# Kernel tuning notes

Measured on AMD Instinct MI355X. Metric: run time of the kernel, lower is better.

Reference implementation:

```python
import jax, jax.numpy as jnp
import numpy as np

B, S, D = 4, 2048, 1024
H = 16
HD = D // H

def setup_inputs() -> dict:
    key = jax.random.key(0)
    ks = jax.random.split(key, 6)
    s = 0.02
    return {
        "input_tensor": jax.random.normal(ks[0], (B, S, D), dtype=jnp.float32),
        "Wq": jax.random.normal(ks[1], (D, D), dtype=jnp.float32) * s,
        "Wk": jax.random.normal(ks[2], (D, D), dtype=jnp.float32) * s,
        "Wv": jax.random.normal(ks[3], (D, D), dtype=jnp.float32) * s,
        "Wo": jax.random.normal(ks[4], (D, D), dtype=jnp.float32) * s,
        "bo": jax.random.normal(ks[5], (D,), dtype=jnp.float32) * s,
    }

def reference(input_tensor, Wq, Wk, Wv, Wo, bo):
    b, n, _ = input_tensor.shape
    # projections (nn.Linear: x @ W.T; bias=False for qkv)
    q = jnp.einsum('bnd,ed->bne', input_tensor, Wq).reshape(b, n, H, HD).transpose(0, 2, 1, 3)
    k = jnp.einsum('bnd,ed->bne', input_tensor, Wk).reshape(b, n, H, HD).transpose(0, 2, 1, 3)
    v = jnp.einsum('bnd,ed->bne', input_tensor, Wv).reshape(b, n, H, HD).transpose(0, 2, 1, 3)
    scores = jnp.einsum('bhqd,bhkd->bhqk', q, k)  # [B,H,S,S]
    causal = jnp.triu(jnp.ones((n, n), dtype=bool), k=1)
    scores = jnp.where(causal, -jnp.inf, scores)
    weights = jax.nn.softmax(scores / jnp.sqrt(jnp.float32(HD)), axis=-1)
    ctx = jnp.einsum('bhqk,bhkd->bhqd', weights, v)  # [B,H,S,HD]
    ctx = ctx.transpose(0, 2, 1, 3).reshape(b, n, D)
    return jnp.einsum('bnd,ed->bne', ctx, Wo) + bo
```

## Files before the change

### kernel.cpp

```cpp
#include <hip/hip_runtime.h>
#include <stdint.h>

#define S_LEN 2048
#define DIM   1024
#define NH    16
#define HD    64
#define BATCH 4
#define M_ROWS (BATCH * S_LEN)
#define PSTR  136

typedef __attribute__((ext_vector_type(8))) __bf16 bf16x8;
typedef __attribute__((ext_vector_type(4))) float  f32x4;

union Frag { bf16x8 v; uint4 q; };

__device__ __forceinline__ ushort f2bf(float f) {
  union { float f; unsigned u; } x; x.f = f;
  unsigned r = x.u + 0x7fffu + ((x.u >> 16) & 1u);
  return (ushort)(r >> 16);
}
__device__ __forceinline__ ushort f2bf_n(float f) {
  union { __bf16 b; ushort u; } x; x.b = (__bf16)f; return x.u;
}

__device__ __forceinline__ f32x4 mfma16(const Frag& a, const Frag& b, f32x4 c) {
  return __builtin_amdgcn_mfma_f32_16x16x32_bf16(a.v, b.v, c, 0, 0, 0);
}

__device__ __forceinline__ void gld_lds16(const ushort* g, ushort* l) {
  __builtin_amdgcn_global_load_lds(
      (__attribute__((address_space(1))) void*)g,
      (__attribute__((address_space(3))) void*)l, 16, 0, 0);
}

__global__ void cast_x_kernel(const float* __restrict__ src, ushort* __restrict__ dst) {
  int i = blockIdx.x * 256 + threadIdx.x;
  float4 f = ((const float4*)src)[i];
  ushort4 u; u.x = f2bf(f.x); u.y = f2bf(f.y); u.z = f2bf(f.z); u.w = f2bf(f.w);
  ((ushort4*)dst)[i] = u;
}

__global__ void cast_w_kernel(const float* __restrict__ w0, const float* __restrict__ w1,
                              const float* __restrict__ w2, const float* __restrict__ w3,
                              ushort* __restrict__ d0, ushort* __restrict__ d1,
                              ushort* __restrict__ d2, ushort* __restrict__ d3) {
  const float* s; ushort* d;
  int z = blockIdx.y;
  if (z == 0) { s = w0; d = d0; } else if (z == 1) { s = w1; d = d1; }
  else if (z == 2) { s = w2; d = d2; } else { s = w3; d = d3; }
  int i = blockIdx.x * 256 + threadIdx.x;
  float4 f = ((const float4*)s)[i];
  ushort4 u; u.x = f2bf(f.x); u.y = f2bf(f.y); u.z = f2bf(f.z); u.w = f2bf(f.w);
  ((ushort4*)d)[i] = u;
}

template <int MODE>
__global__ __launch_bounds__(256)
void gemm_bk64(const ushort* __restrict__ A,
               const ushort* __restrict__ B0, const ushort* __restrict__ B1,
               const ushort* __restrict__ B2,
               ushort* __restrict__ Qb, ushort* __restrict__ Kb, ushort* __restrict__ Vtb,
               float* __restrict__ outf, const float* __restrict__ bias, float scaleq) {
  __shared__ __align__(16) ushort As[128 * 64];
  __shared__ __align__(16) ushort Bs[128 * 64];
  const int K = DIM;
  int lane = threadIdx.x & 63, wave = threadIdx.x >> 6;
  int quad = lane >> 4, l15 = lane & 15;
  int rowBase = blockIdx.y * 128;
  int wsel, colBase;
  const ushort* Bt;
  if (MODE == 0) {
    wsel = blockIdx.x >> 3;
    colBase = (blockIdx.x & 7) * 128;
    Bt = (wsel == 0) ? B0 : (wsel == 1) ? B1 : B2;
  } else {
    wsel = 0;
    colBase = blockIdx.x * 128;
    Bt = B0;
  }
  int wm = (wave >> 1) * 64, wn = (wave & 1) * 64;

  const ushort* Ag = A + (size_t)rowBase * K;
  const ushort* Bg = Bt + (size_t)colBase * K;

  f32x4 acc[4][4];
#pragma unroll
  for (int i = 0; i < 4; i++)
#pragma unroll
    for (int j = 0; j < 4; j++) acc[i][j] = (f32x4){0.f, 0.f, 0.f, 0.f};

  for (int k0 = 0; k0 < K; k0 += 64) {
#pragma unroll
    for (int cc = 0; cc < 4; ++cc) {
      int c = wave * 4 + cc;
      int s = c * 64 + lane;
      int row = s >> 3;
      int c8 = (s & 7) ^ (row & 7);
      gld_lds16(Ag + (size_t)row * K + k0 + c8 * 8, &As[c * 512]);
      gld_lds16(Bg + (size_t)row * K + k0 + c8 * 8, &Bs[c * 512]);
    }
    __syncthreads();
    Frag af[4][2], bf[4][2];
#pragma unroll
    for (int t = 0; t < 4; t++) {
      int ar = wm + t * 16 + l15;
      int br = wn + t * 16 + l15;
#pragma unroll
      for (int kk = 0; kk < 2; kk++) {
        af[t][kk].q = *(const uint4*)&As[ar * 64 + (((kk * 4 + quad) ^ (ar & 7))) * 8];
        bf[t][kk].q = *(const uint4*)&Bs[br * 64 + (((kk * 4 + quad) ^ (br & 7))) * 8];
      }
    }
#pragma unroll
    for (int kk = 0; kk < 2; kk++)
#pragma unroll
      for (int i = 0; i < 4; i++)
#pragma unroll
        for (int j = 0; j < 4; j++) acc[i][j] = mfma16(af[i][kk], bf[j][kk], acc[i][j]);
    __syncthreads();
  }

#pragma unroll
  for (int i = 0; i < 4; i++) {
    int rowt = wm + i * 16 + quad * 4;
#pragma unroll
    for (int j = 0; j < 4; j++) {
      int e = colBase + wn + j * 16 + l15;
      if (MODE == 0) {
        int h = e >> 6, hd = e & 63;
        if (wsel < 2) {
          ushort* dst = wsel ? Kb : Qb;
          float sc = wsel ? 1.f : scaleq;
#pragma unroll
          for (int r = 0; r < 4; r++) {
            int m = rowBase + rowt + r;
            int b = m >> 11, s = m & (S_LEN - 1);
            dst[((size_t)((b * NH + h) * S_LEN + s) << 6) + hd] = f2bf(acc[i][j][r] * sc);
          }
        } else {
          int m0 = rowBase + rowt;
          int b = m0 >> 11, s0 = m0 & (S_LEN - 1);
          ushort4 u;
          u.x = f2bf(acc[i][j][0]); u.y = f2bf(acc[i][j][1]);
          u.z = f2bf(acc[i][j][2]); u.w = f2bf(acc[i][j][3]);
          *(ushort4*)&Vtb[((size_t)((b * NH + h) * HD + hd) << 11) + s0] = u;
        }
      } else {
        float bv = bias[e];
#pragma unroll
        for (int r = 0; r < 4; r++) {
          int m = rowBase + rowt + r;
          outf[(size_t)m * DIM + e] = acc[i][j][r] + bv;
        }
      }
    }
  }
}

__global__ __launch_bounds__(256)
void flash_attn(const ushort* __restrict__ Qb, const ushort* __restrict__ Kb,
                const ushort* __restrict__ Vtb, ushort* __restrict__ Ctx) {
  __shared__ __align__(16) ushort Ks[128 * 64];
  __shared__ __align__(16) ushort Vs[64 * 128];
  __shared__ __align__(16) ushort Ps[4][16 * PSTR];

  int lane = threadIdx.x & 63, wave = threadIdx.x >> 6;
  int quad = lane >> 4, l15 = lane & 15;
  int bh = blockIdx.x;
  int qt = (gridDim.y - 1) - blockIdx.y;
  int q0 = qt * 128, wq0 = wave * 32;

  const ushort* Qh = Qb + (size_t)bh * S_LEN * HD;
  const ushort* Kh = Kb + (size_t)bh * S_LEN * HD;
  const ushort* Vh = Vtb + (size_t)bh * HD * S_LEN;

#pragma unroll
  for (int cc = 0; cc < 4; ++cc) {
    int c = wave * 4 + cc;
    int s = c * 64 + lane;
    int row = s >> 3;
    int c8 = (s & 7) ^ (row & 7);
    gld_lds16(Qh + (size_t)(q0 + row) * HD + c8 * 8, &Ks[c * 512]);
  }
  __syncthreads();
  Frag qf[2][2];
#pragma unroll
  for (int it = 0; it < 2; ++it)
#pragma unroll
    for (int ks = 0; ks < 2; ++ks) {
      int row = wq0 + it * 16 + l15;
      int c8 = (ks * 4 + quad) ^ (row & 7);
      qf[it][ks].q = *(const uint4*)&Ks[row * 64 + c8 * 8];
    }
  __syncthreads();

  float lst[2] = {0.f, 0.f};
  f32x4 oacc[2][4];
#pragma unroll
  for (int it = 0; it < 2; ++it)
#pragma unroll
    for (int dt = 0; dt < 4; ++dt) oacc[it][dt] = (f32x4){0.f, 0.f, 0.f, 0.f};

  ushort* Pw = Ps[wave];

  for (int kt = 0; kt <= qt; ++kt) {
#pragma unroll
    for (int cc = 0; cc < 4; ++cc) {
      int c = wave * 4 + cc;
      int s = c * 64 + lane;
      int krow = s >> 3;
      int kc8 = (s & 7) ^ (krow & 7);
      gld_lds16(Kh + (size_t)(kt * 128 + krow) * HD + kc8 * 8, &Ks[c * 512]);
      int vrow = s >> 4;
      int vc8 = (s & 15) ^ (vrow & 15);
      gld_lds16(Vh + (size_t)vrow * S_LEN + kt * 128 + vc8 * 8, &Vs[c * 512]);
    }
    __syncthreads();

    f32x4 sacc[2][8];
#pragma unroll
    for (int jt = 0; jt < 8; ++jt) {
      int row = jt * 16 + l15;
      Frag kf0, kf1;
      kf0.q = *(const uint4*)&Ks[row * 64 + ((quad) ^ (row & 7)) * 8];
      kf1.q = *(const uint4*)&Ks[row * 64 + ((4 + quad) ^ (row & 7)) * 8];
#pragma unroll
      for (int it = 0; it < 2; ++it) {
        f32x4 a = (f32x4){0.f, 0.f, 0.f, 0.f};
        a = mfma16(kf0, qf[it][0], a);
        a = mfma16(kf1, qf[it][1], a);
        sacc[it][jt] = a;
      }
    }

    if (kt == qt) {
#pragma unroll
      for (int it = 0; it < 2; ++it)
#pragma unroll
        for (int jt = 0; jt < 8; ++jt)
#pragma unroll
          for (int r = 0; r < 4; ++r)
            if (jt * 16 + quad * 4 + r > wq0 + it * 16 + l15)
              sacc[it][jt][r] = -1e30f;
    }

#pragma unroll
    for (int it = 0; it < 2; ++it) {
      float ps = 0.f;
#pragma unroll
      for (int jt = 0; jt < 8; ++jt) {
        float p0 = exp2f(sacc[it][jt][0]);
        float p1 = exp2f(sacc[it][jt][1]);
        float p2 = exp2f(sacc[it][jt][2]);
        float p3 = exp2f(sacc[it][jt][3]);
        ps += (p0 + p1) + (p2 + p3);
        ushort4 u; u.x = f2bf_n(p0); u.y = f2bf_n(p1); u.z = f2bf_n(p2); u.w = f2bf_n(p3);
        *(ushort4*)&Pw[l15 * PSTR + jt * 16 + quad * 4] = u;
      }
      ps += __shfl_xor(ps, 16);
      ps += __shfl_xor(ps, 32);
      lst[it] += ps;

      Frag pf[4];
#pragma unroll
      for (int ks = 0; ks < 4; ++ks)
        pf[ks].q = *(const uint4*)&Pw[l15 * PSTR + ks * 32 + quad * 8];

#pragma unroll
      for (int dt = 0; dt < 4; ++dt) {
        f32x4 a = oacc[it][dt];
#pragma unroll
        for (int ks = 0; ks < 4; ++ks) {
          int row = dt * 16 + l15;
          Frag vf;
          vf.q = *(const uint4*)&Vs[row * 128 + (((ks * 4 + quad) ^ (row & 15))) * 8];
          a = mfma16(pf[ks], vf, a);
        }
        oacc[it][dt] = a;
      }
    }
    __syncthreads();
  }

  int b = bh >> 4, h = bh & 15;
#pragma unroll
  for (int it = 0; it < 2; ++it) {
    float linv = 1.f / lst[it];
    float lr[4];
#pragma unroll
    for (int r = 0; r < 4; ++r) lr[r] = __shfl(linv, quad * 4 + r);
#pragma unroll
    for (int r = 0; r < 4; ++r) {
      int qg = q0 + wq0 + it * 16 + quad * 4 + r;
      size_t base = ((size_t)(b * S_LEN + qg)) * DIM + h * HD;
#pragma unroll
      for (int dt = 0; dt < 4; ++dt)
        Ctx[base + dt * 16 + l15] = f2bf_n(oacc[it][dt][r] * lr[r]);
    }
  }
}

extern "C" void kernel_launch(void* const* d_in, const int* in_sizes, int n_in,
                              void* d_out, int out_size, void* d_ws, size_t ws_size,
                              hipStream_t stream) {
  (void)in_sizes; (void)n_in; (void)out_size; (void)ws_size;
  const float* x  = (const float*)d_in[0];
  const float* Wq = (const float*)d_in[1];
  const float* Wk = (const float*)d_in[2];
  const float* Wv = (const float*)d_in[3];
  const float* Wo = (const float*)d_in[4];
  const float* bo = (const float*)d_in[5];
  float* out = (float*)d_out;

  ushort* Xb  = (ushort*)d_ws;
  ushort* Wqb = Xb  + (size_t)M_ROWS * DIM;
  ushort* Wkb = Wqb + (size_t)DIM * DIM;
  ushort* Wvb = Wkb + (size_t)DIM * DIM;
  ushort* Wob = Wvb + (size_t)DIM * DIM;
  ushort* Qb  = Wob + (size_t)DIM * DIM;
  ushort* Kb  = Qb  + (size_t)M_ROWS * DIM;
  ushort* Vtb = Kb  + (size_t)M_ROWS * DIM;
  ushort* Ctx = Vtb + (size_t)M_ROWS * DIM;

  const float SCALE_Q = 0.18033688011112042f;

  cast_x_kernel<<<dim3(M_ROWS * DIM / 1024), 256, 0, stream>>>(x, Xb);
  cast_w_kernel<<<dim3(DIM * DIM / 1024, 4), 256, 0, stream>>>(Wq, Wk, Wv, Wo, Wqb, Wkb, Wvb, Wob);

  gemm_bk64<0><<<dim3(24, 64), 256, 0, stream>>>(Xb, Wqb, Wkb, Wvb, Qb, Kb, Vtb,
                                                 nullptr, nullptr, SCALE_Q);

  flash_attn<<<dim3(BATCH * NH, S_LEN / 128), 256, 0, stream>>>(Qb, Kb, Vtb, Ctx);

  gemm_bk64<1><<<dim3(8, 64), 256, 0, stream>>>(Ctx, Wob, nullptr, nullptr, nullptr, nullptr,
                                                nullptr, out, bo, 1.0f);
}
```

Measured before the change: 271.5 us.

## Double-buffer K/V tiles in flash attention and prefetch next tile during compute

K and V tiles now live in two LDS buffers. The next tile's global-to-LDS loads are issued before computing on the current one, which removes one barrier per iteration and hides load latency behind the MFMA work. The P scratch buffer switches from row padding to an XOR swizzle. V fragments are loaded once per dt and reused across both query sub-tiles, and s_setprio is raised around the MFMA sections. The added buffers raise LDS use to about 80KB per block, and launch_bounds now asks for 2 blocks per CU, which can squeeze the register budget.

```diff
diff --git a/kernel.cpp b/kernel.cpp
--- a/kernel.cpp
+++ b/kernel.cpp
@@ -7,7 +7,6 @@
 #define HD    64
 #define BATCH 4
 #define M_ROWS (BATCH * S_LEN)
-#define PSTR  136
 
 typedef __attribute__((ext_vector_type(8))) __bf16 bf16x8;
 typedef __attribute__((ext_vector_type(4))) float  f32x4;
@@ -157,12 +156,12 @@
   }
 }
 
-__global__ __launch_bounds__(256)
+__global__ __launch_bounds__(256, 2)
 void flash_attn(const ushort* __restrict__ Qb, const ushort* __restrict__ Kb,
                 const ushort* __restrict__ Vtb, ushort* __restrict__ Ctx) {
-  __shared__ __align__(16) ushort Ks[128 * 64];
-  __shared__ __align__(16) ushort Vs[64 * 128];
-  __shared__ __align__(16) ushort Ps[4][16 * PSTR];
+  __shared__ __align__(16) ushort Ks[2][128 * 64];
+  __shared__ __align__(16) ushort Vs[2][64 * 128];
+  __shared__ __align__(16) ushort Ps[4][16 * 128];
 
   int lane = threadIdx.x & 63, wave = threadIdx.x >> 6;
   int quad = lane >> 4, l15 = lane & 15;
@@ -178,11 +177,14 @@
   for (int cc = 0; cc < 4; ++cc) {
     int c = wave * 4 + cc;
     int s = c * 64 + lane;
-    int row = s >> 3;
-    int c8 = (s & 7) ^ (row & 7);
-    gld_lds16(Qh + (size_t)(q0 + row) * HD + c8 * 8, &Ks[c * 512]);
+    int krow = s >> 3, kc8 = (s & 7) ^ (krow & 7);
+    int vrow = s >> 4, vc8 = (s & 15) ^ (vrow & 15);
+    gld_lds16(Qh + (size_t)(q0 + krow) * HD + kc8 * 8, &Ks[1][c * 512]);
+    gld_lds16(Kh + (size_t)krow * HD + kc8 * 8, &Ks[0][c * 512]);
+    gld_lds16(Vh + (size_t)vrow * S_LEN + vc8 * 8, &Vs[0][c * 512]);
   }
   __syncthreads();
+
   Frag qf[2][2];
 #pragma unroll
   for (int it = 0; it < 2; ++it)
@@ -190,7 +192,7 @@
     for (int ks = 0; ks < 2; ++ks) {
       int row = wq0 + it * 16 + l15;
       int c8 = (ks * 4 + quad) ^ (row & 7);
-      qf[it][ks].q = *(const uint4*)&Ks[row * 64 + c8 * 8];
+      qf[it][ks].q = *(const uint4*)&Ks[1][row * 64 + c8 * 8];
     }
   __syncthreads();
 
@@ -202,28 +204,32 @@
     for (int dt = 0; dt < 4; ++dt) oacc[it][dt] = (f32x4){0.f, 0.f, 0.f, 0.f};
 
   ushort* Pw = Ps[wave];
-
+  const int psw = (l15 & 7) << 3;
+
+  int cur = 0;
   for (int kt = 0; kt <= qt; ++kt) {
-#pragma unroll
-    for (int cc = 0; cc < 4; ++cc) {
-      int c = wave * 4 + cc;
-      int s = c * 64 + lane;
-      int krow = s >> 3;
-      int kc8 = (s & 7) ^ (krow & 7);
-      gld_lds16(Kh + (size_t)(kt * 128 + krow) * HD + kc8 * 8, &Ks[c * 512]);
-      int vrow = s >> 4;
-      int vc8 = (s & 15) ^ (vrow & 15);
-      gld_lds16(Vh + (size_t)vrow * S_LEN + kt * 128 + vc8 * 8, &Vs[c * 512]);
-    }
-    __syncthreads();
+    if (kt < qt) {
+#pragma unroll
+      for (int cc = 0; cc < 4; ++cc) {
+        int c = wave * 4 + cc;
+        int s = c * 64 + lane;
+        int krow = s >> 3, kc8 = (s & 7) ^ (krow & 7);
+        int vrow = s >> 4, vc8 = (s & 15) ^ (vrow & 15);
+        gld_lds16(Kh + (size_t)((kt + 1) * 128 + krow) * HD + kc8 * 8, &Ks[cur ^ 1][c * 512]);
+        gld_lds16(Vh + (size_t)vrow * S_LEN + (kt + 1) * 128 + vc8 * 8, &Vs[cur ^ 1][c * 512]);
+      }
+    }
+    const ushort* Kc = Ks[cur];
+    const ushort* Vc = Vs[cur];
 
     f32x4 sacc[2][8];
+    __builtin_amdgcn_s_setprio(1);
 #pragma unroll
     for (int jt = 0; jt < 8; ++jt) {
       int row = jt * 16 + l15;
       Frag kf0, kf1;
-      kf0.q = *(const uint4*)&Ks[row * 64 + ((quad) ^ (row & 7)) * 8];
-      kf1.q = *(const uint4*)&Ks[row * 64 + ((4 + quad) ^ (row & 7)) * 8];
+      kf0.q = *(const uint4*)&Kc[row * 64 + ((quad ^ (row & 7))) * 8];
+      kf1.q = *(const uint4*)&Kc[row * 64 + (((4 + quad) ^ (row & 7))) * 8];
 #pragma unroll
       for (int it = 0; it < 2; ++it) {
         f32x4 a = (f32x4){0.f, 0.f, 0.f, 0.f};
@@ -232,6 +238,7 @@
         sacc[it][jt] = a;
       }
     }
+    __builtin_amdgcn_s_setprio(0);
 
     if (kt == qt) {
 #pragma unroll
@@ -244,6 +251,7 @@
               sacc[it][jt][r] = -1e30f;
     }
 
+    Frag pf[2][4];
 #pragma unroll
     for (int it = 0; it < 2; ++it) {
       float ps = 0.f;
@@ -255,31 +263,36 @@
         float p3 = exp2f(sacc[it][jt][3]);
         ps += (p0 + p1) + (p2 + p3);
         ushort4 u; u.x = f2bf_n(p0); u.y = f2bf_n(p1); u.z = f2bf_n(p2); u.w = f2bf_n(p3);
-        *(ushort4*)&Pw[l15 * PSTR + jt * 16 + quad * 4] = u;
+        *(ushort4*)&Pw[l15 * 128 + ((jt * 16 + quad * 4) ^ psw)] = u;
       }
       ps += __shfl_xor(ps, 16);
       ps += __shfl_xor(ps, 32);
       lst[it] += ps;
-
-      Frag pf[4];
 #pragma unroll
       for (int ks = 0; ks < 4; ++ks)
-        pf[ks].q = *(const uint4*)&Pw[l15 * PSTR + ks * 32 + quad * 8];
-
-#pragma unroll
-      for (int dt = 0; dt < 4; ++dt) {
+        pf[it][ks].q = *(const uint4*)&Pw[l15 * 128 + ((ks * 32 + quad * 8) ^ psw)];
+    }
+
+    __builtin_amdgcn_s_setprio(1);
+#pragma unroll
+    for (int dt = 0; dt < 4; ++dt) {
+      int row = dt * 16 + l15;
+      Frag vf[4];
+#pragma unroll
+      for (int ks = 0; ks < 4; ++ks)
+        vf[ks].q = *(const uint4*)&Vc[row * 128 + (((ks * 4 + quad) ^ (row & 15))) * 8];
+#pragma unroll
+      for (int it = 0; it < 2; ++it) {
         f32x4 a = oacc[it][dt];
 #pragma unroll
-        for (int ks = 0; ks < 4; ++ks) {
-          int row = dt * 16 + l15;
-          Frag vf;
-          vf.q = *(const uint4*)&Vs[row * 128 + (((ks * 4 + quad) ^ (row & 15))) * 8];
-          a = mfma16(pf[ks], vf, a);
-        }
+        for (int ks = 0; ks < 4; ++ks) a = mfma16(pf[it][ks], vf[ks], a);
         oacc[it][dt] = a;
       }
     }
+    __builtin_amdgcn_s_setprio(0);
+
     __syncthreads();
+    cur ^= 1;
   }
 
   int b = bh >> 4, h = bh & 15;
```

Result: faster. 256.1 us (-5.7%).

## Replace LDS round-trip for P with in-register permlane swaps and reorder tiles

Applied to the files above, without the earlier changes.

The flash-attention kernel no longer stages the softmax probabilities through shared memory. It packs them to bf16 and rearranges them into the MFMA A-operand layout with v_permlane32/16_swap instructions, and it computes the row sums with the same swaps instead of shuffles. V fragments are now loaded once per dt and reused across both query sub-tiles. The change also adds s_setprio around the MFMA sections, an occupancy hint of 4 in launch_bounds, and a balanced q-tile ordering across blockIdx.y. The aim is to remove LDS write/read traffic and waitcnts on P, to cut redundant V loads, and to balance causal work across blocks. The cost is higher register pressure and reliance on gfx950-specific permlane instructions.

```diff
diff --git a/kernel.cpp b/kernel.cpp
--- a/kernel.cpp
+++ b/kernel.cpp
@@ -7,7 +7,6 @@
 #define HD    64
 #define BATCH 4
 #define M_ROWS (BATCH * S_LEN)
-#define PSTR  136
 
 typedef __attribute__((ext_vector_type(8))) __bf16 bf16x8;
 typedef __attribute__((ext_vector_type(4))) float  f32x4;
@@ -157,17 +156,17 @@
   }
 }
 
-__global__ __launch_bounds__(256)
+__global__ __launch_bounds__(256, 4)
 void flash_attn(const ushort* __restrict__ Qb, const ushort* __restrict__ Kb,
                 const ushort* __restrict__ Vtb, ushort* __restrict__ Ctx) {
   __shared__ __align__(16) ushort Ks[128 * 64];
   __shared__ __align__(16) ushort Vs[64 * 128];
-  __shared__ __align__(16) ushort Ps[4][16 * PSTR];
 
   int lane = threadIdx.x & 63, wave = threadIdx.x >> 6;
   int quad = lane >> 4, l15 = lane & 15;
   int bh = blockIdx.x;
-  int qt = (gridDim.y - 1) - blockIdx.y;
+  int yq = blockIdx.y >> 2, yr = blockIdx.y & 3;
+  int qt = (yq == 0) ? (15 - yr) : (yq == 1) ? (8 + yr) : (yq == 2) ? (4 + yr) : (3 - yr);
   int q0 = qt * 128, wq0 = wave * 32;
 
   const ushort* Qh = Qb + (size_t)bh * S_LEN * HD;
@@ -201,84 +200,93 @@
 #pragma unroll
     for (int dt = 0; dt < 4; ++dt) oacc[it][dt] = (f32x4){0.f, 0.f, 0.f, 0.f};
 
-  ushort* Pw = Ps[wave];
-
   for (int kt = 0; kt <= qt; ++kt) {
 #pragma unroll
     for (int cc = 0; cc < 4; ++cc) {
       int c = wave * 4 + cc;
       int s = c * 64 + lane;
-      int krow = s >> 3;
-      int kc8 = (s & 7) ^ (krow & 7);
+      int krow = s >> 3, kc8 = (s & 7) ^ (krow & 7);
+      int vrow = s >> 4, vc8 = (s & 15) ^ (vrow & 15);
       gld_lds16(Kh + (size_t)(kt * 128 + krow) * HD + kc8 * 8, &Ks[c * 512]);
-      int vrow = s >> 4;
-      int vc8 = (s & 15) ^ (vrow & 15);
       gld_lds16(Vh + (size_t)vrow * S_LEN + kt * 128 + vc8 * 8, &Vs[c * 512]);
     }
     __syncthreads();
 
-    f32x4 sacc[2][8];
+    uint sw[2][8][2];
+    float ps[2] = {0.f, 0.f};
+    __builtin_amdgcn_s_setprio(1);
 #pragma unroll
     for (int jt = 0; jt < 8; ++jt) {
       int row = jt * 16 + l15;
       Frag kf0, kf1;
-      kf0.q = *(const uint4*)&Ks[row * 64 + ((quad) ^ (row & 7)) * 8];
-      kf1.q = *(const uint4*)&Ks[row * 64 + ((4 + quad) ^ (row & 7)) * 8];
+      kf0.q = *(const uint4*)&Ks[row * 64 + ((quad ^ (row & 7))) * 8];
+      kf1.q = *(const uint4*)&Ks[row * 64 + (((4 + quad) ^ (row & 7))) * 8];
 #pragma unroll
       for (int it = 0; it < 2; ++it) {
         f32x4 a = (f32x4){0.f, 0.f, 0.f, 0.f};
         a = mfma16(kf0, qf[it][0], a);
         a = mfma16(kf1, qf[it][1], a);
-        sacc[it][jt] = a;
-      }
-    }
-
-    if (kt == qt) {
-#pragma unroll
-      for (int it = 0; it < 2; ++it)
-#pragma unroll
-        for (int jt = 0; jt < 8; ++jt)
+        if (kt == qt) {
 #pragma unroll
           for (int r = 0; r < 4; ++r)
-            if (jt * 16 + quad * 4 + r > wq0 + it * 16 + l15)
-              sacc[it][jt][r] = -1e30f;
-    }
+            if (jt * 16 + quad * 4 + r > wq0 + it * 16 + l15) a[r] = -1e30f;
+        }
+        float p0 = exp2f(a[0]);
+        float p1 = exp2f(a[1]);
+        float p2 = exp2f(a[2]);
+        float p3 = exp2f(a[3]);
+        ps[it] += (p0 + p1) + (p2 + p3);
+        union { ushort2 h; uint u; } w0, w1;
+        w0.h.x = f2bf_n(p0); w0.h.y = f2bf_n(p1);
+        w1.h.x = f2bf_n(p2); w1.h.y = f2bf_n(p3);
+        sw[it][jt][0] = w0.u;
+        sw[it][jt][1] = w1.u;
+      }
+    }
+    __builtin_amdgcn_s_setprio(0);
+
+    Frag pf[2][4];
+#pragma unroll
+    for (int it = 0; it < 2; ++it)
+#pragma unroll
+      for (int ks = 0; ks < 4; ++ks) {
+        uint x0 = sw[it][2 * ks][0], y0 = sw[it][2 * ks + 1][0];
+        uint x1 = sw[it][2 * ks][1], y1 = sw[it][2 * ks + 1][1];
+        asm("v_permlane32_swap_b32 %0, %1" : "+v"(x0), "+v"(y0));
+        asm("v_permlane16_swap_b32 %0, %1" : "+v"(x0), "+v"(y0));
+        asm("v_permlane32_swap_b32 %0, %1" : "+v"(x1), "+v"(y1));
+        asm("v_permlane16_swap_b32 %0, %1" : "+v"(x1), "+v"(y1));
+        pf[it][ks].q = (uint4){x0, x1, y0, y1};
+      }
 
 #pragma unroll
     for (int it = 0; it < 2; ++it) {
-      float ps = 0.f;
-#pragma unroll
-      for (int jt = 0; jt < 8; ++jt) {
-        float p0 = exp2f(sacc[it][jt][0]);
-        float p1 = exp2f(sacc[it][jt][1]);
-        float p2 = exp2f(sacc[it][jt][2]);
-        float p3 = exp2f(sacc[it][jt][3]);
-        ps += (p0 + p1) + (p2 + p3);
-        ushort4 u; u.x = f2bf_n(p0); u.y = f2bf_n(p1); u.z = f2bf_n(p2); u.w = f2bf_n(p3);
-        *(ushort4*)&Pw[l15 * PSTR + jt * 16 + quad * 4] = u;
-      }
-      ps += __shfl_xor(ps, 16);
-      ps += __shfl_xor(ps, 32);
-      lst[it] += ps;
-
-      Frag pf[4];
+      float a = ps[it], b = ps[it];
+      asm("v_permlane32_swap_b32 %0, %1" : "+v"(a), "+v"(b));
+      float s2 = a + b;
+      a = s2; b = s2;
+      asm("v_permlane16_swap_b32 %0, %1" : "+v"(a), "+v"(b));
+      lst[it] += a + b;
+    }
+
+    __builtin_amdgcn_s_setprio(1);
+#pragma unroll
+    for (int dt = 0; dt < 4; ++dt) {
+      int row = dt * 16 + l15;
+      Frag vf[4];
 #pragma unroll
       for (int ks = 0; ks < 4; ++ks)
-        pf[ks].q = *(const uint4*)&Pw[l15 * PSTR + ks * 32 + quad * 8];
-
-#pragma unroll
-      for (int dt = 0; dt < 4; ++dt) {
+        vf[ks].q = *(const uint4*)&Vs[row * 128 + (((ks * 4 + quad) ^ (row & 15))) * 8];
+#pragma unroll
+      for (int it = 0; it < 2; ++it) {
         f32x4 a = oacc[it][dt];
 #pragma unroll
-        for (int ks = 0; ks < 4; ++ks) {
-          int row = dt * 16 + l15;
-          Frag vf;
-          vf.q = *(const uint4*)&Vs[row * 128 + (((ks * 4 + quad) ^ (row & 15))) * 8];
-          a = mfma16(pf[ks], vf, a);
-        }
+        for (int ks = 0; ks < 4; ++ks) a = mfma16(pf[it][ks], vf[ks], a);
         oacc[it][dt] = a;
       }
     }
+    __builtin_amdgcn_s_setprio(0);
+
     __syncthreads();
   }
 
```

New measurement: 301.6 us. 1.11x slower.
